# Optimization experiments

Measured on AMD Instinct MI355X. Metric: run time of the kernel, lower is better.

Reference implementation:

```python
import jax, jax.numpy as jnp
import numpy as np

N_COMP = 16  # sedenion components

def _cd_table(n):
    """Cayley-Dickson basis multiplication table: e_i * e_j = sign[i,j] * e_{idx[i,j]}."""
    if n == 1:
        return np.array([[1]], dtype=np.int64), np.array([[0]], dtype=np.int64)
    m = n // 2
    s, k = _cd_table(m)
    conj = np.where(np.arange(m) == 0, 1, -1)  # conj(e_0)=e_0, conj(e_i)=-e_i
    S = np.zeros((n, n), dtype=np.int64)
    K = np.zeros((n, n), dtype=np.int64)
    for i in range(n):
        for j in range(n):
            if i < m and j < m:          # (a,0)(c,0) = (ac, 0)
                S[i, j] = s[i, j]; K[i, j] = k[i, j]
            elif i < m:                  # (a,0)(0,d) = (0, d a)
                q = j - m
                S[i, j] = s[q, i]; K[i, j] = m + k[q, i]
            elif j < m:                  # (0,b)(c,0) = (0, b c*)
                p = i - m
                S[i, j] = s[p, j] * conj[j]; K[i, j] = m + k[p, j]
            else:                        # (0,b)(0,d) = (-d* b, 0)
                p, q = i - m, j - m
                S[i, j] = -conj[q] * s[q, p]; K[i, j] = k[q, p]
    return S, K

SIGN, IDX = _cd_table(N_COMP)

def _sedenion_kernel(w_comp):
    """Assemble the (16n, 16n) real matrix of the sedenion linear map from 16 (n,n) component weights."""
    blocks = [[None] * N_COMP for _ in range(N_COMP)]
    for i in range(N_COMP):
        for j in range(N_COMP):
            blocks[j][int(IDX[i, j])] = float(SIGN[i, j]) * w_comp[i]
    return jnp.concatenate([jnp.concatenate(row, axis=1) for row in blocks], axis=0)


def setup_inputs() -> dict:
    key = jax.random.key(0)
    k1, k2, k3, k4 = jax.random.split(key, 4)
    B, C, H, W = 8, 96, 256, 256
    x = jax.random.normal(k1, (B, C, H, W), jnp.float32)
    w_comp = jax.random.normal(k2, (N_COMP, C, C), jnp.float32) * 0.02
    proj_w = jax.random.normal(k3, (C, C), jnp.float32) * 0.02
    proj_b = jax.random.normal(k4, (C,), jnp.float32) * 0.02
    return {"x": x, "w_comp": w_comp, "proj_w": proj_w, "proj_b": proj_b}


def reference(x, w_comp, proj_w, proj_b):
    B, C, H, W = x.shape
    h, w = H // 4, W // 4
    # get_window: 'b c (h s1) (w s2) -> b h w (s1 s2 c)' with s1=s2=4
    xw = x.reshape(B, C, h, 4, w, 4).transpose(0, 2, 4, 3, 5, 1).reshape(B, h, w, 16 * C)
    big = _sedenion_kernel(w_comp)          # (16C, 16C)
    y = xw @ big                            # sedenion linear on windowed features
    # reverse_window + 'b c h w -> b h w c' fused: (B,h,w,16C) -> (B,H,W,C)
    y = y.reshape(B, h, w, 4, 4, C).transpose(0, 1, 3, 2, 4, 5).reshape(B, H, W, C)
    y = jax.nn.gelu(y, approximate=False)   # nn.GELU (exact); dropouts are identity (p=0)
    y = y @ proj_w.T + proj_b               # nn.Linear(dim, dim)
    return y.transpose(0, 3, 1, 2)          # 'b h w c -> b c h w'
```

## Files before the change

### kernel.cpp

```cpp
#include <hip/hip_runtime.h>
#include <hip/hip_bf16.h>

typedef __attribute__((ext_vector_type(8))) short short8v;
typedef __attribute__((ext_vector_type(4))) float float4v;

struct SedTab { signed char sgn[256]; signed char idx[256]; };

__device__ inline unsigned short f2bf(float f) {
    __hip_bfloat16 h = __float2bfloat16(f);
    return *reinterpret_cast<unsigned short*>(&h);
}
__device__ inline float bf2f(unsigned short u) {
    union { unsigned int i; float f; } x; x.i = ((unsigned)u) << 16; return x.f;
}

#define GLOAD_LDS16(g, l) __builtin_amdgcn_global_load_lds( \
    (const __attribute__((address_space(1))) void*)(g), \
    (__attribute__((address_space(3))) void*)(l), 16, 0, 0)

__global__ __launch_bounds__(256) void build_bigT(
    const float* __restrict__ w_comp, unsigned short* __restrict__ bigT, SedTab tab)
{
    int e = blockIdx.x * 256 + threadIdx.x;
    if (e >= 1536 * 1536) return;
    int n = e / 1536, k = e - n * 1536;
    int t_out = n / 96, c = n - t_out * 96;
    int t_in = k / 96, m = k - t_in * 96;
    int i = tab.idx[t_in * 16 + t_out];
    float s = (float)tab.sgn[t_in * 16 + t_out];
    float v = s * w_comp[(i * 96 + m) * 96 + c];
    bigT[e] = f2bf(v);
}

__global__ __launch_bounds__(256) void window_cast(
    const float* __restrict__ x, unsigned short* __restrict__ xw)
{
    __shared__ unsigned short lds[96][260];
    int blk = blockIdx.x;
    int s1 = blk & 3, hh = (blk >> 2) & 63, b = blk >> 8;
    const float* src = x + (size_t)b * 6291456 + (size_t)(4 * hh + s1) * 256;

    for (int i = threadIdx.x; i < 6144; i += 256) {
        int m = i >> 6;
        int q = (i & 63) << 2;
        float4 v = *(const float4*)(src + (size_t)m * 65536 + q);
        lds[m][q + 0] = f2bf(v.x);
        lds[m][q + 1] = f2bf(v.y);
        lds[m][q + 2] = f2bf(v.z);
        lds[m][q + 3] = f2bf(v.w);
    }
    __syncthreads();
    size_t rowbase = (size_t)((b * 64 + hh) * 64) * 1536 + (size_t)s1 * 384;
    for (int i = threadIdx.x; i < 3072; i += 256) {
        int ww = i / 48, g = i - ww * 48;
        int s2 = g / 12, mg = (g - s2 * 12) * 8;
        int qq = 4 * ww + s2;
        short8v pk;
        #pragma unroll
        for (int j = 0; j < 8; ++j) pk[j] = (short)lds[mg + j][qq];
        *(short8v*)(xw + rowbase + (size_t)ww * 1536 + s2 * 96 + mg) = pk;
    }
}

__global__ __launch_bounds__(256, 2) void gemm_sed(
    const unsigned short* __restrict__ A,
    const unsigned short* __restrict__ Bt,
    unsigned short* __restrict__ Yg)
{
    __shared__ unsigned short As[128 * 64];
    __shared__ unsigned short Bs[128 * 64];
    const int t = threadIdx.x;
    const int lane = t & 63;
    const int w = t >> 6;
    const int wm = w >> 1, wn = w & 1;
    const int mt = blockIdx.x / 12, nt = blockIdx.x - mt * 12;
    const int m0 = mt * 128, n0 = nt * 128;
    const int lr = lane & 15;
    const int lk = (lane >> 4) << 3;

    float4v acc[4][4];
    #pragma unroll
    for (int i = 0; i < 4; ++i)
        #pragma unroll
        for (int j = 0; j < 4; ++j) acc[i][j] = (float4v)0.0f;

    for (int k0 = 0; k0 < 1536; k0 += 64) {
        __syncthreads();
        #pragma unroll
        for (int i = 0; i < 4; ++i) {
            const int c = t + i * 256;
            const int row = c >> 3, kc = (c & 7) << 3;
            GLOAD_LDS16(A + (size_t)(m0 + row) * 1536 + k0 + kc, (char*)As + c * 16);
            GLOAD_LDS16(Bt + (size_t)(n0 + row) * 1536 + k0 + kc, (char*)Bs + c * 16);
        }
        __syncthreads();
        #pragma unroll
        for (int kk = 0; kk < 64; kk += 32) {
            short8v af[4], bf[4];
            #pragma unroll
            for (int f = 0; f < 4; ++f)
                af[f] = *(const short8v*)(As + (wm * 64 + f * 16 + lr) * 64 + kk + lk);
            #pragma unroll
            for (int f = 0; f < 4; ++f)
                bf[f] = *(const short8v*)(Bs + (wn * 64 + f * 16 + lr) * 64 + kk + lk);
            #pragma unroll
            for (int mf = 0; mf < 4; ++mf)
                #pragma unroll
                for (int nf = 0; nf < 4; ++nf)
                    acc[mf][nf] = __builtin_amdgcn_mfma_f32_16x16x32_bf16(
                        af[mf], bf[nf], acc[mf][nf], 0, 0, 0);
        }
    }

    #pragma unroll
    for (int mf = 0; mf < 4; ++mf) {
        #pragma unroll
        for (int r = 0; r < 4; ++r) {
            const int gm = m0 + wm * 64 + mf * 16 + (lane >> 4) * 4 + r;
            #pragma unroll
            for (int nf = 0; nf < 4; ++nf) {
                const int gn = n0 + wn * 64 + nf * 16 + lr;
                float v = acc[mf][nf][r];
                float g = 0.5f * v * (1.0f + erff(v * 0.70710678118654752f));
                Yg[(size_t)gm * 1536 + gn] = f2bf(g);
            }
        }
    }
}

__global__ __launch_bounds__(256, 2) void proj_mfma(
    const unsigned short* __restrict__ Yg,
    const float* __restrict__ pw, const float* __restrict__ pb,
    float* __restrict__ out)
{
    __shared__ unsigned short gys[256 * 104];
    __shared__ unsigned short pws[96 * 104];
    __shared__ float pbs[96];

    const int blk = blockIdx.x;
    const int s1 = blk & 3, hh = (blk >> 2) & 63, b = blk >> 8;
    const int t = threadIdx.x;
    const int lane = t & 63, w = t >> 6;
    const int lr = lane & 15;

    for (int i = t; i < 9216; i += 256) {
        int r = i / 96, c = i - r * 96;
        pws[r * 104 + c] = f2bf(pw[i]);
    }
    if (t < 96) pbs[t] = pb[t];

    size_t rowbase = (size_t)((b * 64 + hh) * 64) * 1536 + (size_t)s1 * 384;
    for (int i = t; i < 3072; i += 256) {
        int ww = i / 48, v = i - ww * 48;
        short8v pk = *(const short8v*)(Yg + rowbase + (size_t)ww * 1536 + v * 8);
        int s2 = v / 12;
        int c = (v - s2 * 12) * 8;
        int q = 4 * ww + s2;
        *(short8v*)(&gys[q * 104 + c]) = pk;
    }
    __syncthreads();

    float4v acc[6][4];
    #pragma unroll
    for (int i = 0; i < 6; ++i)
        #pragma unroll
        for (int j = 0; j < 4; ++j) acc[i][j] = (float4v)0.0f;

    #pragma unroll
    for (int ks = 0; ks < 3; ++ks) {
        const int lk = ks * 32 + ((lane >> 4) << 3);
        short8v af[6], bf[4];
        #pragma unroll
        for (int mf = 0; mf < 6; ++mf)
            af[mf] = *(const short8v*)(&pws[(mf * 16 + lr) * 104 + lk]);
        #pragma unroll
        for (int nf = 0; nf < 4; ++nf)
            bf[nf] = *(const short8v*)(&gys[(w * 64 + nf * 16 + lr) * 104 + lk]);
        #pragma unroll
        for (int mf = 0; mf < 6; ++mf)
            #pragma unroll
            for (int nf = 0; nf < 4; ++nf)
                acc[mf][nf] = __builtin_amdgcn_mfma_f32_16x16x32_bf16(
                    af[mf], bf[nf], acc[mf][nf], 0, 0, 0);
    }

    const int p = 4 * hh + s1;
    const size_t obase = (size_t)b * 6291456 + (size_t)p * 256;
    #pragma unroll
    for (int mf = 0; mf < 6; ++mf) {
        #pragma unroll
        for (int r = 0; r < 4; ++r) {
            const int c = mf * 16 + (lane >> 4) * 4 + r;
            const float bias = pbs[c];
            #pragma unroll
            for (int nf = 0; nf < 4; ++nf) {
                const int q = w * 64 + nf * 16 + lr;
                out[obase + (size_t)c * 65536 + q] = acc[mf][nf][r] + bias;
            }
        }
    }
}

static void cd_table(int n, int* S, int* K) {
    if (n == 1) { S[0] = 1; K[0] = 0; return; }
    int m = n / 2;
    int s[64], k[64];
    cd_table(m, s, k);
    for (int i = 0; i < n; ++i) {
        for (int j = 0; j < n; ++j) {
            if (i < m && j < m) { S[i*n+j] = s[i*m+j]; K[i*n+j] = k[i*m+j]; }
            else if (i < m) { int q = j - m; S[i*n+j] = s[q*m+i]; K[i*n+j] = m + k[q*m+i]; }
            else if (j < m) { int p = i - m; int cj = (j == 0) ? 1 : -1;
                              S[i*n+j] = s[p*m+j] * cj; K[i*n+j] = m + k[p*m+j]; }
            else { int p = i - m, q = j - m; int cq = (q == 0) ? 1 : -1;
                   S[i*n+j] = -cq * s[q*m+p]; K[i*n+j] = k[q*m+p]; }
        }
    }
}

extern "C" void kernel_launch(void* const* d_in, const int* in_sizes, int n_in,
                              void* d_out, int out_size, void* d_ws, size_t ws_size,
                              hipStream_t stream) {
    const float* x      = (const float*)d_in[0];
    const float* w_comp = (const float*)d_in[1];
    const float* proj_w = (const float*)d_in[2];
    const float* proj_b = (const float*)d_in[3];
    float* out = (float*)d_out;

    unsigned short* BigT = (unsigned short*)d_ws;
    unsigned short* Yg   = (unsigned short*)((char*)d_ws + 4718592);
    unsigned short* Xw   = (unsigned short*)d_out;

    int S16[256], K16[256];
    cd_table(16, S16, K16);
    SedTab tab;
    for (int i = 0; i < 16; ++i)
        for (int j = 0; j < 16; ++j) {
            int k = K16[i * 16 + j];
            tab.idx[j * 16 + k] = (signed char)i;
            tab.sgn[j * 16 + k] = (signed char)S16[i * 16 + j];
        }

    hipLaunchKernelGGL(build_bigT, dim3(9216), dim3(256), 0, stream, w_comp, BigT, tab);
    hipLaunchKernelGGL(window_cast, dim3(2048), dim3(256), 0, stream, x, Xw);
    hipLaunchKernelGGL(gemm_sed, dim3(3072), dim3(256), 0, stream, Xw, BigT, Yg);
    hipLaunchKernelGGL(proj_mfma, dim3(2048), dim3(256), 0, stream, Yg, proj_w, proj_b, out);
}
```

Before: 350.0 us.

## Rewrite main GEMM as 8-wave 128x256 tile with triple-buffered LDS pipeline

The sedenion GEMM now uses 512-thread blocks with 128x256 output tiles. It triple-buffers LDS via async global-to-LDS loads issued two k-steps ahead, using explicit vmcnt waits. LDS columns are XOR-swizzled to avoid bank conflicts, each k-step is split into two MFMA phases with s_setprio, and blocks are remapped across XCDs for L2 locality. The aim is to hide global load latency and raise MFMA utilization, at the cost of more LDS (144KB per block) and fragile hand-ordered barriers and waitcounts.

```diff
diff --git a/kernel.cpp b/kernel.cpp
--- a/kernel.cpp
+++ b/kernel.cpp
@@ -17,6 +17,8 @@
 #define GLOAD_LDS16(g, l) __builtin_amdgcn_global_load_lds( \
     (const __attribute__((address_space(1))) void*)(g), \
     (__attribute__((address_space(3))) void*)(l), 16, 0, 0)
+
+#define VMCNT(n) asm volatile("s_waitcnt vmcnt(" #n ")" ::: "memory")
 
 __global__ __launch_bounds__(256) void build_bigT(
     const float* __restrict__ w_comp, unsigned short* __restrict__ bigT, SedTab tab)
@@ -62,21 +64,22 @@
     }
 }
 
-__global__ __launch_bounds__(256, 2) void gemm_sed(
+__global__ __launch_bounds__(512, 2) void gemm_sed8(
     const unsigned short* __restrict__ A,
     const unsigned short* __restrict__ Bt,
     unsigned short* __restrict__ Yg)
 {
-    __shared__ unsigned short As[128 * 64];
-    __shared__ unsigned short Bs[128 * 64];
+    __shared__ unsigned short As[3][128 * 64];
+    __shared__ unsigned short Bs[3][256 * 64];
     const int t = threadIdx.x;
-    const int lane = t & 63;
-    const int w = t >> 6;
-    const int wm = w >> 1, wn = w & 1;
-    const int mt = blockIdx.x / 12, nt = blockIdx.x - mt * 12;
-    const int m0 = mt * 128, n0 = nt * 128;
-    const int lr = lane & 15;
-    const int lk = (lane >> 4) << 3;
+    const int lane = t & 63, w = t >> 6;
+    const int wm = w >> 2, wn = w & 3;
+    const int lr = lane & 15, lg = lane >> 4;
+
+    const int bid = blockIdx.x;
+    const int wg = (bid & 7) * 192 + (bid >> 3);
+    const int nt = wg >> 8, mt = wg & 255;
+    const int m0 = mt * 128, n0 = nt * 256;
 
     float4v acc[4][4];
     #pragma unroll
@@ -84,39 +87,98 @@
         #pragma unroll
         for (int j = 0; j < 4; ++j) acc[i][j] = (float4v)0.0f;
 
-    for (int k0 = 0; k0 < 1536; k0 += 64) {
-        __syncthreads();
-        #pragma unroll
-        for (int i = 0; i < 4; ++i) {
-            const int c = t + i * 256;
-            const int row = c >> 3, kc = (c & 7) << 3;
-            GLOAD_LDS16(A + (size_t)(m0 + row) * 1536 + k0 + kc, (char*)As + c * 16);
-            GLOAD_LDS16(Bt + (size_t)(n0 + row) * 1536 + k0 + kc, (char*)Bs + c * 16);
-        }
-        __syncthreads();
-        #pragma unroll
-        for (int kk = 0; kk < 64; kk += 32) {
-            short8v af[4], bf[4];
-            #pragma unroll
-            for (int f = 0; f < 4; ++f)
-                af[f] = *(const short8v*)(As + (wm * 64 + f * 16 + lr) * 64 + kk + lk);
-            #pragma unroll
-            for (int f = 0; f < 4; ++f)
-                bf[f] = *(const short8v*)(Bs + (wn * 64 + f * 16 + lr) * 64 + kk + lk);
+    auto stageA = [&](int kt, int slot, int i) {
+        const int c = t + i * 512;
+        const int row = c >> 3;
+        const int kc = (((c & 7) ^ (row & 7)) << 3);
+        GLOAD_LDS16(A + (size_t)(m0 + row) * 1536 + kt * 64 + kc,
+                    (char*)&As[slot][0] + c * 16);
+    };
+    auto stageB = [&](int kt, int slot, int i) {
+        const int c = t + i * 512;
+        const int row = c >> 3;
+        const int kc = (((c & 7) ^ (row & 7)) << 3);
+        GLOAD_LDS16(Bt + (size_t)(n0 + row) * 1536 + kt * 64 + kc,
+                    (char*)&Bs[slot][0] + c * 16);
+    };
+
+    stageA(0, 0, 0); stageA(0, 0, 1);
+    stageB(0, 0, 0); stageB(0, 0, 1); stageB(0, 0, 2); stageB(0, 0, 3);
+    stageA(1, 1, 0); stageA(1, 1, 1);
+    stageB(1, 1, 0); stageB(1, 1, 1); stageB(1, 1, 2); stageB(1, 1, 3);
+    VMCNT(6);
+    __builtin_amdgcn_s_barrier();
+
+    int slot = 0;
+    for (int kt = 0; kt < 24; ++kt) {
+        const int ps = (slot == 0) ? 2 : slot - 1;
+        const int pf = kt + 2;
+        const bool st = (pf < 24);
+
+        short8v a[4][2], b0[2][2];
+        #pragma unroll
+        for (int mf = 0; mf < 4; ++mf)
+            #pragma unroll
+            for (int ks = 0; ks < 2; ++ks) {
+                const int row = wm * 64 + mf * 16 + lr;
+                const int col = (ks * 32 + lg * 8) ^ ((row & 7) << 3);
+                a[mf][ks] = *(const short8v*)(&As[slot][row * 64 + col]);
+            }
+        #pragma unroll
+        for (int nf = 0; nf < 2; ++nf)
+            #pragma unroll
+            for (int ks = 0; ks < 2; ++ks) {
+                const int row = wn * 64 + nf * 16 + lr;
+                const int col = (ks * 32 + lg * 8) ^ ((row & 7) << 3);
+                b0[nf][ks] = *(const short8v*)(&Bs[slot][row * 64 + col]);
+            }
+        if (st) { stageA(pf, ps, 0); stageA(pf, ps, 1); stageB(pf, ps, 0); }
+        __builtin_amdgcn_s_barrier();
+        __builtin_amdgcn_s_setprio(1);
+        #pragma unroll
+        for (int ks = 0; ks < 2; ++ks)
             #pragma unroll
             for (int mf = 0; mf < 4; ++mf)
                 #pragma unroll
-                for (int nf = 0; nf < 4; ++nf)
+                for (int nf = 0; nf < 2; ++nf)
                     acc[mf][nf] = __builtin_amdgcn_mfma_f32_16x16x32_bf16(
-                        af[mf], bf[nf], acc[mf][nf], 0, 0, 0);
-        }
+                        a[mf][ks], b0[nf][ks], acc[mf][nf], 0, 0, 0);
+        __builtin_amdgcn_s_setprio(0);
+        __builtin_amdgcn_s_barrier();
+
+        short8v b1[2][2];
+        #pragma unroll
+        for (int nf = 0; nf < 2; ++nf)
+            #pragma unroll
+            for (int ks = 0; ks < 2; ++ks) {
+                const int row = wn * 64 + (nf + 2) * 16 + lr;
+                const int col = (ks * 32 + lg * 8) ^ ((row & 7) << 3);
+                b1[nf][ks] = *(const short8v*)(&Bs[slot][row * 64 + col]);
+            }
+        if (st) { stageB(pf, ps, 1); stageB(pf, ps, 2); stageB(pf, ps, 3); }
+        if (kt < 22)       { VMCNT(6); }
+        else if (kt == 22) { VMCNT(0); }
+        __builtin_amdgcn_s_barrier();
+        __builtin_amdgcn_s_setprio(1);
+        #pragma unroll
+        for (int ks = 0; ks < 2; ++ks)
+            #pragma unroll
+            for (int mf = 0; mf < 4; ++mf)
+                #pragma unroll
+                for (int nf = 0; nf < 2; ++nf)
+                    acc[mf][nf + 2] = __builtin_amdgcn_mfma_f32_16x16x32_bf16(
+                        a[mf][ks], b1[nf][ks], acc[mf][nf + 2], 0, 0, 0);
+        __builtin_amdgcn_s_setprio(0);
+        __builtin_amdgcn_s_barrier();
+
+        slot = (slot == 2) ? 0 : slot + 1;
     }
 
     #pragma unroll
     for (int mf = 0; mf < 4; ++mf) {
         #pragma unroll
         for (int r = 0; r < 4; ++r) {
-            const int gm = m0 + wm * 64 + mf * 16 + (lane >> 4) * 4 + r;
+            const int gm = m0 + wm * 64 + mf * 16 + lg * 4 + r;
             #pragma unroll
             for (int nf = 0; nf < 4; ++nf) {
                 const int gn = n0 + wn * 64 + nf * 16 + lr;
@@ -243,6 +305,6 @@
 
     hipLaunchKernelGGL(build_bigT, dim3(9216), dim3(256), 0, stream, w_comp, BigT, tab);
     hipLaunchKernelGGL(window_cast, dim3(2048), dim3(256), 0, stream, x, Xw);
-    hipLaunchKernelGGL(gemm_sed, dim3(3072), dim3(256), 0, stream, Xw, BigT, Yg);
+    hipLaunchKernelGGL(gemm_sed8, dim3(1536), dim3(512), 0, stream, Xw, BigT, Yg);
     hipLaunchKernelGGL(proj_mfma, dim3(2048), dim3(256), 0, stream, Yg, proj_w, proj_b, out);
 }
```

New measurement: 364.5 us. 1.04x slower.
